# Kernel tuning notes

Hardware: AMD Instinct MI355X
Metric: run time of the kernel (lower is better)

## Reference

```python
import jax, jax.numpy as jnp
import numpy as np

B, D, M = 64, 256, 100  # batch, reduced channel dim, h*w of feature map (10x10)

# Precompute upper-triangle (including diagonal) flat indices for Triuvec
_r, _c = np.triu_indices(D)
FLAT_TRIU_IDX = jnp.asarray(_r * D + _c)  # [D*(D+1)/2]


def setup_inputs() -> dict:
    key = jax.random.key(0)
    k1, = jax.random.split(key, 1)
    feat_map = jax.random.normal(k1, (B, D, M), dtype=jnp.float32)
    # temperature param init: log(1 / (2 * h * w)) with h = w = 10
    temperature = jnp.full((1, 1), np.log(1.0 / (2 * 10 * 10)), dtype=jnp.float32)
    return {"feat_map": feat_map, "temperature": temperature}


def reference(feat_map, temperature):
    # feat_map: [B, D, M]; temperature: [1, 1] learned scalar
    b, d, m = feat_map.shape
    f1 = feat_map[:, :, None, :]  # [B, D, 1, M]
    f2 = feat_map[:, None, :, :]  # [B, 1, D, M]
    # item_1 - item_2, summed over map dim; idea_variant path: (i1 - i2)/2 * exp(T)
    out = 0.5 * jnp.sum(jnp.abs(f1 + f2) - jnp.abs(f1 - f2), axis=-1)  # [B, D, D]
    out = out * jnp.exp(temperature[0, 0])
    # normalize_bdc double-centering: out - (1/D) out @ 1 - (1/D) 1 @ out
    row = jnp.sum(out, axis=2, keepdims=True) / d  # [B, D, 1]
    col = jnp.sum(out, axis=1, keepdims=True) / d  # [B, 1, D]
    out = out - row - col
    # Triuvec (with diagonal): gather upper-triangle entries
    vec = out.reshape(b, d * d)[:, FLAT_TRIU_IDX]  # [B, D*(D+1)/2]
    return vec
```

## Files before the change

kernel.cpp:

```cpp
#include <hip/hip_runtime.h>


#define NB 64
#define DD 256
#define MM 100
#define TILE 64
#define NUT 10
#define TRI_PER_B 32896
#define NTILE 640
#define NMQ 25
#define TILE_F (TILE * TILE)
#define PSTRIDE 192

typedef unsigned int u32;
typedef _Float16 f16x2 __attribute__((ext_vector_type(2)));

__device__ __forceinline__ void tile_coords(int t, int& ti, int& tj) {
    int a = (t >= 4) + (t >= 7) + (t >= 9);
    int s = (a * (9 - a)) >> 1;
    ti = a;
    tj = t - s + a;
}

__device__ __forceinline__ u32 slot_enc(int g) {
    return g == 0 ? 0x03020100u : g == 1 ? 0x21060504u
         : g == 2 ? 0x25220807u : 0x28262309u;
}

extern "C" __global__ void __launch_bounds__(256, 5)
k_partial(const float* __restrict__ f, float* __restrict__ part,
          _Float16* __restrict__ tiles) {
    __shared__ u32 As[NMQ][TILE][2];
    __shared__ u32 Bs[NMQ][32][2];
    const int t = threadIdx.x;
    const int unit = (blockIdx.x & 7) * 160 + (blockIdx.x >> 3);
    const int bt = unit >> 1;
    const int half = unit & 1;
    const int b = bt / NUT;
    const int ut = bt % NUT;
    int ti, tj;
    tile_coords(ut, ti, tj);
    const int i0 = ti * TILE;
    const int j0 = tj * TILE + half * 32;
    const float* fb = f + (size_t)b * DD * MM;

    for (int l = t; l < TILE * NMQ; l += 256) {
        const int il = l & 63;
        const int mq = l >> 6;
        float4 v = *reinterpret_cast<const float4*>(fb + (size_t)(i0 + il) * MM + mq * 4);
        uint2 p;
        p.x = __builtin_bit_cast(u32, __builtin_amdgcn_cvt_pkrtz(v.x, v.y));
        p.y = __builtin_bit_cast(u32, __builtin_amdgcn_cvt_pkrtz(v.z, v.w));
        *reinterpret_cast<uint2*>(&As[mq][il][0]) = p;
    }
    for (int l = t; l < 32 * NMQ; l += 256) {
        const int il = l & 31;
        const int mq = l >> 5;
        float4 w = *reinterpret_cast<const float4*>(fb + (size_t)(j0 + il) * MM + mq * 4);
        uint2 p;
        p.x = __builtin_bit_cast(u32, __builtin_amdgcn_cvt_pkrtz(w.x, w.y));
        p.y = __builtin_bit_cast(u32, __builtin_amdgcn_cvt_pkrtz(w.z, w.w));
        *reinterpret_cast<uint2*>(&Bs[mq][il][0]) = p;
    }
    __syncthreads();

    const int cg = t & 15;
    const int rg = t >> 4;
    float acc[4][2] = {};

    const int c0 = (int)(((t >> 6) + blockIdx.x) % 5u);
    for (int cc = 0; cc < 5; ++cc) {
        int ch = c0 + cc;
        if (ch >= 5) ch -= 5;
        const int mqb = ch * 5;
        #pragma unroll
        for (int k = 0; k < 5; ++k) {
            const int mq = mqb + k;
            uint4 alo = *reinterpret_cast<const uint4*>(&As[mq][rg * 4 + 0][0]);
            uint4 ahi = *reinterpret_cast<const uint4*>(&As[mq][rg * 4 + 2][0]);
            uint4 bb  = *reinterpret_cast<const uint4*>(&Bs[mq][cg * 2][0]);
            const u32 al[4] = {alo.x, alo.y, alo.z, alo.w};
            const u32 ah[4] = {ahi.x, ahi.y, ahi.z, ahi.w};
            const u32 bl[4] = {bb.x, bb.y, bb.z, bb.w};
            #pragma unroll
            for (int e = 0; e < 2; ++e) {
                const u32 av[4] = {al[e], al[2 + e], ah[e], ah[2 + e]};
                const u32 bv[2] = {bl[e], bl[2 + e]};
                u32 aab[4], aso[4], bab[2], bsg[2];
                #pragma unroll
                for (int q = 0; q < 4; ++q) {
                    aab[q] = av[q] & 0x7fff7fffu;
                    aso[q] = (av[q] & 0x80008000u) | 0x3c003c00u;
                }
                #pragma unroll
                for (int c = 0; c < 2; ++c) {
                    bab[c] = bv[c] & 0x7fff7fffu;
                    bsg[c] = bv[c] & 0x80008000u;
                }
                #pragma unroll
                for (int q = 0; q < 4; ++q) {
                    #pragma unroll
                    for (int c = 0; c < 2; ++c) {
                        u32 so = aso[q] ^ bsg[c];
                        f16x2 mn = __builtin_elementwise_min(
                            __builtin_bit_cast(f16x2, aab[q]),
                            __builtin_bit_cast(f16x2, bab[c]));
                        acc[q][c] = __builtin_amdgcn_fdot2(
                            mn, __builtin_bit_cast(f16x2, so), acc[q][c], false);
                    }
                }
            }
        }
    }

    _Float16* tp = tiles + (size_t)bt * TILE_F;
    #pragma unroll
    for (int q = 0; q < 4; ++q) {
        *reinterpret_cast<u32*>(tp + (rg * 4 + q) * TILE + half * 32 + cg * 2) =
            __builtin_bit_cast(u32, __builtin_amdgcn_cvt_pkrtz(acc[q][0], acc[q][1]));
    }

    float ra[4], cb[2];
    #pragma unroll
    for (int q = 0; q < 4; ++q) ra[q] = acc[q][0] + acc[q][1];
    #pragma unroll
    for (int c = 0; c < 2; ++c)
        cb[c] = (acc[0][c] + acc[1][c]) + (acc[2][c] + acc[3][c]);

    __syncthreads();
    float* red  = reinterpret_cast<float*>(&As[0][0][0]);
    float* red2 = red + 1024;
    #pragma unroll
    for (int q = 0; q < 4; ++q) red[cg * 64 + rg * 4 + q] = ra[q];
    #pragma unroll
    for (int c = 0; c < 2; ++c) red2[rg * 32 + cg * 2 + c] = cb[c];
    __syncthreads();

    float* pb = part + (size_t)bt * PSTRIDE;
    if (t < TILE) {
        float s = 0.f;
        #pragma unroll
        for (int w = 0; w < 16; ++w) s += red[w * 64 + t];
        pb[half * 64 + t] = s;
    } else if (t < TILE + 32 && ti != tj) {
        const int u = t - TILE;
        float s = 0.f;
        #pragma unroll
        for (int w = 0; w < 16; ++w) s += red2[w * 32 + u];
        pb[128 + half * 32 + u] = s;
    }
}

extern "C" __global__ void __launch_bounds__(256)
k_finalize(const float* __restrict__ part, const float* __restrict__ temp,
           const _Float16* __restrict__ tiles, float* __restrict__ out) {
    __shared__ float rows_sh[128];
    const int t = threadIdx.x;
    const int unit = (blockIdx.x & 7) * 160 + (blockIdx.x >> 3);
    const int bt = unit >> 1;
    const int half = unit & 1;
    const int b = bt / NUT;
    const int ut = bt % NUT;
    int ti, tj;
    tile_coords(ut, ti, tj);
    const int i0 = ti * TILE, j0 = tj * TILE + half * 32;
    const int tix = t >> 4, tiy = t & 15;

    if (t < 96) {
        const int isrow = (t < 64);
        const int u = isrow ? t : (half * 32 + (t - 64));
        const int g = isrow ? ti : tj;
        const u32 enc = slot_enc(g);
        float sum = 0.f;
        #pragma unroll
        for (int s = 0; s < 4; ++s) {
            const u32 byte = (enc >> (8 * s)) & 0xffu;
            const int ut_s = byte & 0x1f;
            const int side = byte >> 5;
            const float* pb = part + (size_t)(b * NUT + ut_s) * PSTRIDE;
            sum += side ? pb[128 + u] : (pb[u] + pb[64 + u]);
        }
        rows_sh[t] = sum;
    }

    const _Float16* tp = tiles + (size_t)bt * TILE_F;
    float vv[4][2];
    #pragma unroll
    for (int q = 0; q < 4; ++q) {
        u32 w = *reinterpret_cast<const u32*>(
            tp + (tix * 4 + q) * TILE + half * 32 + tiy * 2);
        f16x2 hv = __builtin_bit_cast(f16x2, w);
        vv[q][0] = (float)hv.x;
        vv[q][1] = (float)hv.y;
    }
    __syncthreads();

    const float scale = expf(temp[0]);
    const float inv_d = 1.0f / DD;
    float rloc[4], cloc[2];
    #pragma unroll
    for (int q = 0; q < 4; ++q) rloc[q] = rows_sh[tix * 4 + q];
    #pragma unroll
    for (int c = 0; c < 2; ++c) {
        const int lc = tiy * 2 + c;
        cloc[c] = (ti == tj) ? rows_sh[half * 32 + lc] : rows_sh[64 + lc];
    }

    float* ob = out + (size_t)b * TRI_PER_B;
    #pragma unroll
    for (int q = 0; q < 4; ++q) {
        const int i = i0 + tix * 4 + q;
        const int j0e = j0 + tiy * 2;
        float v0 = scale * (vv[q][0] - (rloc[q] + cloc[0]) * inv_d);
        float v1 = scale * (vv[q][1] - (rloc[q] + cloc[1]) * inv_d);
        if (ti != tj) {
            const int off = (i * (2 * DD - i + 1)) / 2 + (j0e - i);
            *reinterpret_cast<float2*>(ob + off) = make_float2(v0, v1);
        } else {
            if (j0e >= i)     ob[(i * (2 * DD - i + 1)) / 2 + (j0e - i)]     = v0;
            if (j0e + 1 >= i) ob[(i * (2 * DD - i + 1)) / 2 + (j0e + 1 - i)] = v1;
        }
    }
}

extern "C" void kernel_launch(void* const* d_in, const int* in_sizes, int n_in,
                              void* d_out, int out_size, void* d_ws, size_t ws_size,
                              hipStream_t stream) {
    const float* f    = (const float*)d_in[0];
    const float* temp = (const float*)d_in[1];
    float* out  = (float*)d_out;
    float* part = (float*)d_ws;
    _Float16* tiles = (_Float16*)(part + NTILE * PSTRIDE);

    k_partial<<<2 * NTILE, 256, 0, stream>>>(f, part, tiles);
    k_finalize<<<2 * NTILE, 256, 0, stream>>>(part, temp, tiles, out);
}
```

Before: 35.81 us.

## Compute full 64x64 tile per 512-thread block instead of half-tiles

k_partial now launches one 512-thread block per 64x64 tile instead of two 256-thread blocks per 32-column half. The A rows are loaded once per tile rather than twice, and the row-sum partials no longer need combining across halves. Shared memory is re-laid out as [50][64] packed half2 pairs, and the rotating chunk order used to spread bank conflicts is dropped. The risks are heavier per-block shared memory and register pressure at 512 threads, and fewer blocks to fill the CUs.

```diff
diff --git a/kernel.cpp b/kernel.cpp
--- a/kernel.cpp
+++ b/kernel.cpp
@@ -8,9 +8,8 @@
 #define NUT 10
 #define TRI_PER_B 32896
 #define NTILE 640
-#define NMQ 25
+#define NM2 50
 #define TILE_F (TILE * TILE)
-#define PSTRIDE 192
 
 typedef unsigned int u32;
 typedef _Float16 f16x2 __attribute__((ext_vector_type(2)));
@@ -27,88 +26,64 @@
          : g == 2 ? 0x25220807u : 0x28262309u;
 }
 
-extern "C" __global__ void __launch_bounds__(256, 5)
+__device__ __forceinline__ int swz_bt(int w) { return (w & 7) * 80 + (w >> 3); }
+
+extern "C" __global__ void __launch_bounds__(512, 5)
 k_partial(const float* __restrict__ f, float* __restrict__ part,
           _Float16* __restrict__ tiles) {
-    __shared__ u32 As[NMQ][TILE][2];
-    __shared__ u32 Bs[NMQ][32][2];
+    __shared__ u32 As[NM2][TILE];
+    __shared__ u32 Bs[NM2][TILE];
     const int t = threadIdx.x;
-    const int unit = (blockIdx.x & 7) * 160 + (blockIdx.x >> 3);
-    const int bt = unit >> 1;
-    const int half = unit & 1;
+    const int bt = swz_bt(blockIdx.x);
     const int b = bt / NUT;
     const int ut = bt % NUT;
     int ti, tj;
     tile_coords(ut, ti, tj);
-    const int i0 = ti * TILE;
-    const int j0 = tj * TILE + half * 32;
+    const int i0 = ti * TILE, j0 = tj * TILE;
     const float* fb = f + (size_t)b * DD * MM;
 
-    for (int l = t; l < TILE * NMQ; l += 256) {
+    for (int l = t; l < TILE * 25; l += 512) {
         const int il = l & 63;
         const int mq = l >> 6;
         float4 v = *reinterpret_cast<const float4*>(fb + (size_t)(i0 + il) * MM + mq * 4);
-        uint2 p;
-        p.x = __builtin_bit_cast(u32, __builtin_amdgcn_cvt_pkrtz(v.x, v.y));
-        p.y = __builtin_bit_cast(u32, __builtin_amdgcn_cvt_pkrtz(v.z, v.w));
-        *reinterpret_cast<uint2*>(&As[mq][il][0]) = p;
-    }
-    for (int l = t; l < 32 * NMQ; l += 256) {
-        const int il = l & 31;
-        const int mq = l >> 5;
+        As[2 * mq + 0][il] = __builtin_bit_cast(u32, __builtin_amdgcn_cvt_pkrtz(v.x, v.y));
+        As[2 * mq + 1][il] = __builtin_bit_cast(u32, __builtin_amdgcn_cvt_pkrtz(v.z, v.w));
         float4 w = *reinterpret_cast<const float4*>(fb + (size_t)(j0 + il) * MM + mq * 4);
-        uint2 p;
-        p.x = __builtin_bit_cast(u32, __builtin_amdgcn_cvt_pkrtz(w.x, w.y));
-        p.y = __builtin_bit_cast(u32, __builtin_amdgcn_cvt_pkrtz(w.z, w.w));
-        *reinterpret_cast<uint2*>(&Bs[mq][il][0]) = p;
-    }
-    __syncthreads();
-
-    const int cg = t & 15;
-    const int rg = t >> 4;
+        Bs[2 * mq + 0][il] = __builtin_bit_cast(u32, __builtin_amdgcn_cvt_pkrtz(w.x, w.y));
+        Bs[2 * mq + 1][il] = __builtin_bit_cast(u32, __builtin_amdgcn_cvt_pkrtz(w.z, w.w));
+    }
+    __syncthreads();
+
+    const int rg = t >> 5, cg = t & 31;
     float acc[4][2] = {};
 
-    const int c0 = (int)(((t >> 6) + blockIdx.x) % 5u);
-    for (int cc = 0; cc < 5; ++cc) {
-        int ch = c0 + cc;
-        if (ch >= 5) ch -= 5;
-        const int mqb = ch * 5;
-        #pragma unroll
-        for (int k = 0; k < 5; ++k) {
-            const int mq = mqb + k;
-            uint4 alo = *reinterpret_cast<const uint4*>(&As[mq][rg * 4 + 0][0]);
-            uint4 ahi = *reinterpret_cast<const uint4*>(&As[mq][rg * 4 + 2][0]);
-            uint4 bb  = *reinterpret_cast<const uint4*>(&Bs[mq][cg * 2][0]);
-            const u32 al[4] = {alo.x, alo.y, alo.z, alo.w};
-            const u32 ah[4] = {ahi.x, ahi.y, ahi.z, ahi.w};
-            const u32 bl[4] = {bb.x, bb.y, bb.z, bb.w};
+    #pragma unroll 5
+    for (int m2 = 0; m2 < NM2; ++m2) {
+        uint4 afu = *reinterpret_cast<const uint4*>(&As[m2][rg * 4]);
+        uint2 bfu = *reinterpret_cast<const uint2*>(&Bs[m2][cg * 2]);
+        const u32 av[4] = {afu.x, afu.y, afu.z, afu.w};
+        const u32 bv[2] = {bfu.x, bfu.y};
+        u32 aab[4], aso[4], bab[2], bsg[2];
+        #pragma unroll
+        for (int q = 0; q < 4; ++q) {
+            aab[q] = av[q] & 0x7fff7fffu;
+            aso[q] = (av[q] & 0x80008000u) | 0x3c003c00u;
+        }
+        #pragma unroll
+        for (int c = 0; c < 2; ++c) {
+            bab[c] = bv[c] & 0x7fff7fffu;
+            bsg[c] = bv[c] & 0x80008000u;
+        }
+        #pragma unroll
+        for (int q = 0; q < 4; ++q) {
             #pragma unroll
-            for (int e = 0; e < 2; ++e) {
-                const u32 av[4] = {al[e], al[2 + e], ah[e], ah[2 + e]};
-                const u32 bv[2] = {bl[e], bl[2 + e]};
-                u32 aab[4], aso[4], bab[2], bsg[2];
-                #pragma unroll
-                for (int q = 0; q < 4; ++q) {
-                    aab[q] = av[q] & 0x7fff7fffu;
-                    aso[q] = (av[q] & 0x80008000u) | 0x3c003c00u;
-                }
-                #pragma unroll
-                for (int c = 0; c < 2; ++c) {
-                    bab[c] = bv[c] & 0x7fff7fffu;
-                    bsg[c] = bv[c] & 0x80008000u;
-                }
-                #pragma unroll
-                for (int q = 0; q < 4; ++q) {
-                    #pragma unroll
-                    for (int c = 0; c < 2; ++c) {
-                        u32 so = aso[q] ^ bsg[c];
-                        f16x2 mn = __builtin_elementwise_min(
-                            __builtin_bit_cast(f16x2, aab[q]),
-                            __builtin_bit_cast(f16x2, bab[c]));
-                        acc[q][c] = __builtin_amdgcn_fdot2(
-                            mn, __builtin_bit_cast(f16x2, so), acc[q][c], false);
-                    }
-                }
+            for (int c = 0; c < 2; ++c) {
+                u32 so = aso[q] ^ bsg[c];
+                f16x2 mn = __builtin_elementwise_min(
+                    __builtin_bit_cast(f16x2, aab[q]),
+                    __builtin_bit_cast(f16x2, bab[c]));
+                acc[q][c] = __builtin_amdgcn_fdot2(
+                    mn, __builtin_bit_cast(f16x2, so), acc[q][c], false);
             }
         }
     }
@@ -116,7 +91,7 @@
     _Float16* tp = tiles + (size_t)bt * TILE_F;
     #pragma unroll
     for (int q = 0; q < 4; ++q) {
-        *reinterpret_cast<u32*>(tp + (rg * 4 + q) * TILE + half * 32 + cg * 2) =
+        *reinterpret_cast<u32*>(tp + (rg * 4 + q) * TILE + cg * 2) =
             __builtin_bit_cast(u32, __builtin_amdgcn_cvt_pkrtz(acc[q][0], acc[q][1]));
     }
 
@@ -128,33 +103,33 @@
         cb[c] = (acc[0][c] + acc[1][c]) + (acc[2][c] + acc[3][c]);
 
     __syncthreads();
-    float* red  = reinterpret_cast<float*>(&As[0][0][0]);
-    float* red2 = red + 1024;
+    float* red  = reinterpret_cast<float*>(&As[0][0]);
+    float* red2 = red + 2048;
     #pragma unroll
     for (int q = 0; q < 4; ++q) red[cg * 64 + rg * 4 + q] = ra[q];
     #pragma unroll
-    for (int c = 0; c < 2; ++c) red2[rg * 32 + cg * 2 + c] = cb[c];
-    __syncthreads();
-
-    float* pb = part + (size_t)bt * PSTRIDE;
+    for (int c = 0; c < 2; ++c) red2[rg * 64 + cg * 2 + c] = cb[c];
+    __syncthreads();
+
+    float* pb = part + (size_t)bt * 128;
     if (t < TILE) {
         float s = 0.f;
         #pragma unroll
-        for (int w = 0; w < 16; ++w) s += red[w * 64 + t];
-        pb[half * 64 + t] = s;
-    } else if (t < TILE + 32 && ti != tj) {
+        for (int w = 0; w < 32; ++w) s += red[w * 64 + t];
+        pb[t] = s;
+    } else if (t < 2 * TILE && ti != tj) {
         const int u = t - TILE;
         float s = 0.f;
         #pragma unroll
-        for (int w = 0; w < 16; ++w) s += red2[w * 32 + u];
-        pb[128 + half * 32 + u] = s;
+        for (int w = 0; w < 16; ++w) s += red2[w * 64 + u];
+        pb[64 + u] = s;
     }
 }
 
 extern "C" __global__ void __launch_bounds__(256)
 k_finalize(const float* __restrict__ part, const float* __restrict__ temp,
            const _Float16* __restrict__ tiles, float* __restrict__ out) {
-    __shared__ float rows_sh[128];
+    __shared__ float rows_sh[96];
     const int t = threadIdx.x;
     const int unit = (blockIdx.x & 7) * 160 + (blockIdx.x >> 3);
     const int bt = unit >> 1;
@@ -177,8 +152,7 @@
             const u32 byte = (enc >> (8 * s)) & 0xffu;
             const int ut_s = byte & 0x1f;
             const int side = byte >> 5;
-            const float* pb = part + (size_t)(b * NUT + ut_s) * PSTRIDE;
-            sum += side ? pb[128 + u] : (pb[u] + pb[64 + u]);
+            sum += part[(size_t)(b * NUT + ut_s) * 128 + side * 64 + u];
         }
         rows_sh[t] = sum;
     }
@@ -230,8 +204,8 @@
     const float* temp = (const float*)d_in[1];
     float* out  = (float*)d_out;
     float* part = (float*)d_ws;
-    _Float16* tiles = (_Float16*)(part + NTILE * PSTRIDE);
-
-    k_partial<<<2 * NTILE, 256, 0, stream>>>(f, part, tiles);
+    _Float16* tiles = (_Float16*)(part + NTILE * 128);
+
+    k_partial<<<NTILE, 512, 0, stream>>>(f, part, tiles);
     k_finalize<<<2 * NTILE, 256, 0, stream>>>(part, temp, tiles, out);
 }
```

Measured after the change: 35.73 us. Within noise of the previous version (-0.2%).
